# Optimization experiments

Measured on AMD Instinct MI355X. Metric: run time of the kernel, lower is better.

## Reference

```python
import jax, jax.numpy as jnp
import numpy as np

EPS = 1e-5
NEG_SLOPE = 0.1


def _gcn_layer(x, row, col, W, b):
    # GCNConv, improved=True (self-loop weight 2.0), symmetric normalization.
    N = x.shape[0]
    xw = x @ W                                   # [N, H]
    ew = jnp.ones(row.shape[0], dtype=x.dtype)   # edge_weight=None -> ones
    deg = jax.ops.segment_sum(ew, col, num_segments=N) + 2.0  # +2 from improved self loop
    dinv = jax.lax.rsqrt(deg)                    # deg >= 2, always finite
    norm = dinv[row] * dinv[col]                 # [E]
    agg = jax.ops.segment_sum(norm[:, None] * xw[row], col, num_segments=N)
    agg = agg + (2.0 * dinv * dinv)[:, None] * xw  # self-loop contribution
    return agg + b


def _batchnorm(x, w, b):
    # training-mode BN over node dim (biased variance), eps=1e-5
    mu = jnp.mean(x, axis=0)
    var = jnp.mean((x - mu) ** 2, axis=0)
    return (x - mu) * jax.lax.rsqrt(var + EPS) * w + b


def setup_inputs() -> dict:
    key = jax.random.key(0)
    ks = jax.random.split(key, 10)
    N, E, F, H, OUT, G = 100000, 800000, 128, 128, 128, 2048
    x = jax.random.normal(ks[0], (N, F), dtype=jnp.float32)
    edge_index = jax.random.randint(ks[1], (2, E), 0, N, dtype=jnp.int64)
    batch = jnp.sort(jax.random.randint(ks[2], (N,), 0, G, dtype=jnp.int64))
    s1 = 1.0 / np.sqrt(F)
    s2 = 1.0 / np.sqrt(H)
    return {
        "x": x,
        "edge_index": edge_index,
        "batch": batch,
        "W1": jax.random.uniform(ks[3], (F, H), jnp.float32, -s1, s1),
        "b1": jnp.zeros((H,), jnp.float32),
        "bn1_w": jnp.ones((H,), jnp.float32),
        "bn1_b": jnp.zeros((H,), jnp.float32),
        "W2": jax.random.uniform(ks[4], (H, H), jnp.float32, -s2, s2),
        "b2": jnp.zeros((H,), jnp.float32),
        "bn2_w": jnp.ones((H,), jnp.float32),
        "bn2_b": jnp.zeros((H,), jnp.float32),
        "Wf": jax.random.uniform(ks[5], (H, OUT), jnp.float32, -s2, s2),
        "bf": jax.random.uniform(ks[6], (OUT,), jnp.float32, -s2, s2),
        "num_graphs": G,
    }


def reference(x, edge_index, batch, W1, b1, bn1_w, bn1_b, W2, b2, bn2_w, bn2_b, Wf, bf, num_graphs):
    row, col = edge_index[0], edge_index[1]
    h = _gcn_layer(x, row, col, W1, b1)
    h = jax.nn.leaky_relu(_batchnorm(h, bn1_w, bn1_b), NEG_SLOPE)
    # dropout omitted (deterministic reference / eval mode)
    h = _gcn_layer(h, row, col, W2, b2)
    h = jax.nn.leaky_relu(_batchnorm(h, bn2_w, bn2_b), NEG_SLOPE)
    pooled = jax.ops.segment_max(h, batch, num_segments=num_graphs)  # [G, H]
    pooled = jnp.where(jnp.isneginf(pooled), 0.0, pooled)            # empty graphs -> 0
    return pooled @ Wf + bf
```

## Files before the change

### kernel.cpp

```cpp
#include <hip/hip_runtime.h>
#include <hip/hip_bf16.h>

#define EPSV 1e-5f
#define SLOPE 0.1f

typedef __attribute__((ext_vector_type(8))) unsigned short ushort8v;

static __device__ inline unsigned short f2bf(float f) {
    __hip_bfloat16 b = __float2bfloat16(f);
    return *reinterpret_cast<unsigned short*>(&b);
}
static __device__ inline float bf2f(unsigned short u) {
    return __uint_as_float(((unsigned)u) << 16);
}

__global__ __launch_bounds__(256) void k_count(const int* __restrict__ col,
                                               unsigned* __restrict__ cnt, int E) {
    int e = blockIdx.x * 256 + threadIdx.x;
    if (e < E) atomicAdd(&cnt[col[e]], 1u);
}

__global__ __launch_bounds__(256) void k_dinv(const unsigned* __restrict__ cnt,
                                              float* __restrict__ dinv, int N) {
    int n = blockIdx.x * 256 + threadIdx.x;
    if (n < N) dinv[n] = rsqrtf((float)cnt[n] + 2.0f);
}

__global__ __launch_bounds__(256) void k_chunk_sum(const unsigned* __restrict__ cnt, int N,
                                                   unsigned* __restrict__ bsum) {
    __shared__ unsigned ls[256];
    int base = blockIdx.x * 1024;
    unsigned s = 0;
    for (int i = threadIdx.x; i < 1024; i += 256) {
        int idx = base + i;
        if (idx < N) s += cnt[idx];
    }
    ls[threadIdx.x] = s;
    __syncthreads();
    for (int st = 128; st > 0; st >>= 1) {
        if (threadIdx.x < st) ls[threadIdx.x] += ls[threadIdx.x + st];
        __syncthreads();
    }
    if (threadIdx.x == 0) bsum[blockIdx.x] = ls[0];
}

__global__ void k_scan_bsum(unsigned* __restrict__ bsum, int nb) {
    if (threadIdx.x == 0 && blockIdx.x == 0) {
        unsigned acc = 0;
        for (int i = 0; i < nb; i++) { unsigned v = bsum[i]; bsum[i] = acc; acc += v; }
    }
}

__global__ __launch_bounds__(256) void k_scan_chunks(const unsigned* __restrict__ cnt, int N,
                                                     const unsigned* __restrict__ bsum,
                                                     int* __restrict__ off, int E) {
    __shared__ unsigned ls[256];
    int base = blockIdx.x * 1024;
    unsigned v[4];
    unsigned s = 0;
#pragma unroll
    for (int j = 0; j < 4; j++) {
        int idx = base + threadIdx.x * 4 + j;
        v[j] = (idx < N) ? cnt[idx] : 0u;
        s += v[j];
    }
    ls[threadIdx.x] = s;
    __syncthreads();
    if (threadIdx.x == 0) {
        unsigned acc = bsum[blockIdx.x];
        for (int i = 0; i < 256; i++) { unsigned t = ls[i]; ls[i] = acc; acc += t; }
    }
    __syncthreads();
    unsigned acc = ls[threadIdx.x];
#pragma unroll
    for (int j = 0; j < 4; j++) {
        int idx = base + threadIdx.x * 4 + j;
        if (idx < N) off[idx] = (int)acc;
        acc += v[j];
    }
    if (base + threadIdx.x * 4 <= N - 1 && N - 1 < base + threadIdx.x * 4 + 4) off[N] = E;
}

__global__ __launch_bounds__(256) void k_place(const int* __restrict__ row,
                                               const int* __restrict__ col,
                                               const float* __restrict__ dinv,
                                               int* __restrict__ cursor,
                                               int2* __restrict__ spack, int E) {
    int e = blockIdx.x * 256 + threadIdx.x;
    if (e >= E) return;
    int r = row[e], c = col[e];
    int pos = atomicAdd(&cursor[c], 1);
    spack[pos] = make_int2(r, __float_as_int(dinv[r] * dinv[c]));
}

template <int MODE>
__global__ __launch_bounds__(256) void k_gemm_t(const float* __restrict__ X,
                                                const float* __restrict__ W,
                                                const float* __restrict__ sums, float invN,
                                                const float* __restrict__ bnw,
                                                const float* __restrict__ bnb,
                                                const float* __restrict__ bias,
                                                void* __restrict__ Yv, int N) {
    __shared__ float xs[64][132];
    __shared__ float sc[128], sb[128];
    const int tid = threadIdx.x;
    if (MODE == 1) {
        if (tid < 128) {
            float mu = sums[tid] * invN;
            float var = sums[128 + tid] * invN - mu * mu;
            float s = rsqrtf(var + EPSV) * bnw[tid];
            sc[tid] = s;
            sb[tid] = bnb[tid] - mu * s;
        }
        __syncthreads();
    }
    const int base = blockIdx.x * 64;
    for (int i = tid; i < 2048; i += 256) {
        int r = i >> 5, c4 = i & 31;
        int row = base + r; if (row >= N) row = N - 1;
        float4 v = ((const float4*)(X + (size_t)row * 128))[c4];
        if (MODE == 1) {
            int f = c4 * 4;
            v.x = fmaf(v.x, sc[f + 0], sb[f + 0]); v.x = v.x > 0.f ? v.x : SLOPE * v.x;
            v.y = fmaf(v.y, sc[f + 1], sb[f + 1]); v.y = v.y > 0.f ? v.y : SLOPE * v.y;
            v.z = fmaf(v.z, sc[f + 2], sb[f + 2]); v.z = v.z > 0.f ? v.z : SLOPE * v.z;
            v.w = fmaf(v.w, sc[f + 3], sb[f + 3]); v.w = v.w > 0.f ? v.w : SLOPE * v.w;
        }
        *(float4*)(&xs[r][c4 * 4]) = v;
    }
    __syncthreads();
    const int c0 = (tid & 31) * 4;
    const int rg = tid >> 5;
    float acc[8][4];
#pragma unroll
    for (int i = 0; i < 8; i++) { acc[i][0] = acc[i][1] = acc[i][2] = acc[i][3] = 0.f; }
    for (int k = 0; k < 128; k += 4) {
        float4 w0 = *(const float4*)(W + (size_t)(k + 0) * 128 + c0);
        float4 w1 = *(const float4*)(W + (size_t)(k + 1) * 128 + c0);
        float4 w2 = *(const float4*)(W + (size_t)(k + 2) * 128 + c0);
        float4 w3 = *(const float4*)(W + (size_t)(k + 3) * 128 + c0);
#pragma unroll
        for (int i = 0; i < 8; i++) {
            float4 a = *(const float4*)(&xs[rg + 8 * i][k]);
            acc[i][0] = fmaf(a.x, w0.x, fmaf(a.y, w1.x, fmaf(a.z, w2.x, fmaf(a.w, w3.x, acc[i][0]))));
            acc[i][1] = fmaf(a.x, w0.y, fmaf(a.y, w1.y, fmaf(a.z, w2.y, fmaf(a.w, w3.y, acc[i][1]))));
            acc[i][2] = fmaf(a.x, w0.z, fmaf(a.y, w1.z, fmaf(a.z, w2.z, fmaf(a.w, w3.z, acc[i][2]))));
            acc[i][3] = fmaf(a.x, w0.w, fmaf(a.y, w1.w, fmaf(a.z, w2.w, fmaf(a.w, w3.w, acc[i][3]))));
        }
    }
#pragma unroll
    for (int i = 0; i < 8; i++) {
        int row = base + rg + 8 * i;
        if (row < N) {
            if (MODE == 2) {
                float4 o = make_float4(acc[i][0] + bias[c0], acc[i][1] + bias[c0 + 1],
                                       acc[i][2] + bias[c0 + 2], acc[i][3] + bias[c0 + 3]);
                ((float4*)((float*)Yv + (size_t)row * 128))[tid & 31] = o;
            } else {
                ushort4 o;
                o.x = f2bf(acc[i][0]); o.y = f2bf(acc[i][1]);
                o.z = f2bf(acc[i][2]); o.w = f2bf(acc[i][3]);
                ((ushort4*)((unsigned short*)Yv + (size_t)row * 128))[tid & 31] = o;
            }
        }
    }
}

__global__ __launch_bounds__(256) void k_agg2(const unsigned short* __restrict__ xwh,
                                              const int* __restrict__ off,
                                              const int2* __restrict__ spack,
                                              const float* __restrict__ dinv,
                                              const float* __restrict__ bias,
                                              float* __restrict__ h,
                                              float* __restrict__ sums, int N) {
    __shared__ float ls1[128], ls2[128];
    const int tid = threadIdx.x;
    if (tid < 128) { ls1[tid] = 0.f; ls2[tid] = 0.f; }
    __syncthreads();

    const int lane = tid & 63;
    const int q = lane & 15;
    const int g = lane >> 4;
    const int wave = blockIdx.x * 4 + (tid >> 6);
    const int nW = gridDim.x * 4;

    float st1[8] = {0, 0, 0, 0, 0, 0, 0, 0};
    float st2[8] = {0, 0, 0, 0, 0, 0, 0, 0};
    float bj[8];
#pragma unroll
    for (int j = 0; j < 8; j++) bj[j] = bias[q * 8 + j];

    for (int n = wave; n < N; n += nW) {
        int s = off[n], e = off[n + 1];
        float a[8] = {0, 0, 0, 0, 0, 0, 0, 0};
        int i = s + g;
        if (i < e) {
            int2 p = spack[i];
            while (true) {
                int inext = i + 4;
                bool more = inext < e;
                int2 pn = make_int2(0, 0);
                if (more) pn = spack[inext];
                float nm = __int_as_float(p.y);
                ushort8v v = *(const ushort8v*)(xwh + (size_t)p.x * 128 + q * 8);
#pragma unroll
                for (int j = 0; j < 8; j++) a[j] = fmaf(nm, bf2f(v[j]), a[j]);
                if (!more) break;
                p = pn; i = inext;
            }
        }
#pragma unroll
        for (int j = 0; j < 8; j++) {
            a[j] += __shfl_xor(a[j], 16);
            a[j] += __shfl_xor(a[j], 32);
        }
        if (lane < 16) {
            float dc = dinv[n];
            float sl = 2.f * dc * dc;
            ushort8v xv = *(const ushort8v*)(xwh + (size_t)n * 128 + q * 8);
            float o[8];
#pragma unroll
            for (int j = 0; j < 8; j++) {
                o[j] = a[j] + sl * bf2f(xv[j]) + bj[j];
                st1[j] += o[j];
                st2[j] += o[j] * o[j];
            }
            float4* hp = (float4*)(h + (size_t)n * 128 + q * 8);
            hp[0] = make_float4(o[0], o[1], o[2], o[3]);
            hp[1] = make_float4(o[4], o[5], o[6], o[7]);
        }
    }
    if (lane < 16) {
#pragma unroll
        for (int j = 0; j < 8; j++) {
            atomicAdd(&ls1[q * 8 + j], st1[j]);
            atomicAdd(&ls2[q * 8 + j], st2[j]);
        }
    }
    __syncthreads();
    if (tid < 128) {
        atomicAdd(&sums[tid], ls1[tid]);
        atomicAdd(&sums[128 + tid], ls2[tid]);
    }
}

__global__ __launch_bounds__(256) void k_pool_init(unsigned* __restrict__ p, int total) {
    int i = blockIdx.x * 256 + threadIdx.x;
    if (i < total) p[i] = 0x007FFFFFu;
}

__device__ inline unsigned enc_f(float x) {
    unsigned u = __float_as_uint(x);
    return (u & 0x80000000u) ? ~u : (u | 0x80000000u);
}

__global__ __launch_bounds__(256) void k_pool2(const float* __restrict__ h,
                                               const int* __restrict__ batch,
                                               const float* __restrict__ sums, float invN,
                                               const float* __restrict__ bnw,
                                               const float* __restrict__ bnb,
                                               unsigned* __restrict__ pooled, int N) {
    const int f = threadIdx.x & 127;
    const int half = threadIdx.x >> 7;
    float mu = sums[f] * invN;
    float var = sums[128 + f] * invN - mu * mu;
    float scale = rsqrtf(var + EPSV) * bnw[f];
    float bias = bnb[f] - mu * scale;
    const int base = blockIdx.x * 128;
    const int end = min(base + 128, N);
    float m = -__builtin_inff();
    int g = -1;
    for (int n = base + half; n < end; n += 2) {
        int bg = batch[n];
        if (bg != g) {
            if (g >= 0) atomicMax(&pooled[(size_t)g * 128 + f], enc_f(m));
            g = bg;
            m = -__builtin_inff();
        }
        float v = fmaf(h[(size_t)n * 128 + f], scale, bias);
        v = v > 0.f ? v : SLOPE * v;
        m = fmaxf(m, v);
    }
    if (g >= 0) atomicMax(&pooled[(size_t)g * 128 + f], enc_f(m));
}

__global__ __launch_bounds__(256) void k_decode(unsigned* __restrict__ p, int total) {
    int i = blockIdx.x * 256 + threadIdx.x;
    if (i >= total) return;
    unsigned u = p[i];
    float v;
    if (u == 0x007FFFFFu) v = 0.f;
    else if (u & 0x80000000u) v = __uint_as_float(u & 0x7FFFFFFFu);
    else v = __uint_as_float(~u);
    p[i] = __float_as_uint(v);
}

extern "C" void kernel_launch(void* const* d_in, const int* in_sizes, int n_in,
                              void* d_out, int out_size, void* d_ws, size_t ws_size,
                              hipStream_t stream) {
    const float* x     = (const float*)d_in[0];
    const int*   ei    = (const int*)d_in[1];
    const int*   batch = (const int*)d_in[2];
    const float* W1    = (const float*)d_in[3];
    const float* b1    = (const float*)d_in[4];
    const float* bn1w  = (const float*)d_in[5];
    const float* bn1b  = (const float*)d_in[6];
    const float* W2    = (const float*)d_in[7];
    const float* b2    = (const float*)d_in[8];
    const float* bn2w  = (const float*)d_in[9];
    const float* bn2b  = (const float*)d_in[10];
    const float* Wf    = (const float*)d_in[11];
    const float* bf    = (const float*)d_in[12];

    const int N = in_sizes[0] / 128;
    const int E = in_sizes[1] / 2;
    const int G = out_size / 128;
    const int* rowp = ei;
    const int* colp = ei + E;
    float* out = (float*)d_out;
    const float invN = 1.0f / N;

    char* w = (char*)d_ws;
    unsigned short* bufAh = (unsigned short*)w; w += (size_t)N * 128 * 2;
    float*    bufB   = (float*)w;    w += (size_t)N * 128 * 4;
    float*    dinv   = (float*)w;    w += (size_t)N * 4;
    unsigned* cnt    = (unsigned*)w; w += (size_t)N * 4;
    int*      off    = (int*)w;      w += (size_t)(N + 1) * 4;
    unsigned* bsum   = (unsigned*)w; w += 1024 * 4;
    int2*     spack  = (int2*)w;     w += (size_t)E * 8;
    float*    sums   = (float*)w;    w += 512 * 4;
    unsigned* pooled = (unsigned*)w; w += (size_t)G * 128 * 4;

    float* sums1 = sums;
    float* sums2 = sums + 256;
    const int nb = (N + 1023) / 1024;

    hipMemsetAsync(cnt, 0, (size_t)N * 4, stream);
    hipMemsetAsync(sums, 0, 512 * 4, stream);
    k_count<<<(E + 255) / 256, 256, 0, stream>>>(colp, cnt, E);
    k_dinv<<<(N + 255) / 256, 256, 0, stream>>>(cnt, dinv, N);
    k_chunk_sum<<<nb, 256, 0, stream>>>(cnt, N, bsum);
    k_scan_bsum<<<1, 64, 0, stream>>>(bsum, nb);
    k_scan_chunks<<<nb, 256, 0, stream>>>(cnt, N, bsum, off, E);
    hipMemcpyAsync(cnt, off, (size_t)N * 4, hipMemcpyDeviceToDevice, stream);
    k_place<<<(E + 255) / 256, 256, 0, stream>>>(rowp, colp, dinv, (int*)cnt, spack, E);

    k_gemm_t<0><<<(N + 63) / 64, 256, 0, stream>>>(x, W1, nullptr, 0.f, nullptr, nullptr,
                                                   nullptr, bufAh, N);
    k_agg2<<<2048, 256, 0, stream>>>(bufAh, off, spack, dinv, b1, bufB, sums1, N);

    k_gemm_t<1><<<(N + 63) / 64, 256, 0, stream>>>(bufB, W2, sums1, invN, bn1w, bn1b,
                                                   nullptr, bufAh, N);
    k_agg2<<<2048, 256, 0, stream>>>(bufAh, off, spack, dinv, b2, bufB, sums2, N);

    k_pool_init<<<(G * 128 + 255) / 256, 256, 0, stream>>>(pooled, G * 128);
    k_pool2<<<(N + 127) / 128, 256, 0, stream>>>(bufB, batch, sums2, invN, bn2w, bn2b,
                                                 pooled, N);
    k_decode<<<(G * 128 + 255) / 256, 256, 0, stream>>>(pooled, G * 128);

    k_gemm_t<2><<<(G + 63) / 64, 256, 0, stream>>>((const float*)pooled, Wf, nullptr, 0.f,
                                                   nullptr, nullptr, bf, out, G);
}
```

Baseline: 507.3 us.

## Aggregate edges per node-block with shared-memory atomics instead of wave-per-node

Replaces the wave-per-node gather aggregation with a block-per-64-nodes scheme. Each block streams its whole contiguous CSR edge range in 16-edge groups and accumulates into a 64x128 LDS tile using workgroup-scope float atomics. A second pass in the same block adds the self-loop and bias, writes h and reduces BN statistics. This balances work across edges regardless of per-node degree and removes the per-node shuffle reduction. In exchange it doubles the packed edge record to 16 bytes to carry the destination node, adds LDS atomic contention, and uses 32KB of shared memory per block, which limits occupancy.

```diff
diff --git a/kernel.cpp b/kernel.cpp
--- a/kernel.cpp
+++ b/kernel.cpp
@@ -3,6 +3,7 @@
 
 #define EPSV 1e-5f
 #define SLOPE 0.1f
+#define NB 64
 
 typedef __attribute__((ext_vector_type(8))) unsigned short ushort8v;
 
@@ -85,12 +86,12 @@
                                                const int* __restrict__ col,
                                                const float* __restrict__ dinv,
                                                int* __restrict__ cursor,
-                                               int2* __restrict__ spack, int E) {
+                                               int4* __restrict__ spack, int E) {
     int e = blockIdx.x * 256 + threadIdx.x;
     if (e >= E) return;
     int r = row[e], c = col[e];
     int pos = atomicAdd(&cursor[c], 1);
-    spack[pos] = make_int2(r, __float_as_int(dinv[r] * dinv[c]));
+    spack[pos] = make_int4(r, __float_as_int(dinv[r] * dinv[c]), c, 0);
 }
 
 template <int MODE>
@@ -166,81 +167,69 @@
     }
 }
 
-__global__ __launch_bounds__(256) void k_agg2(const unsigned short* __restrict__ xwh,
+__global__ __launch_bounds__(256) void k_agg3(const unsigned short* __restrict__ xwh,
                                               const int* __restrict__ off,
-                                              const int2* __restrict__ spack,
+                                              const int4* __restrict__ spack,
                                               const float* __restrict__ dinv,
                                               const float* __restrict__ bias,
                                               float* __restrict__ h,
                                               float* __restrict__ sums, int N) {
-    __shared__ float ls1[128], ls2[128];
+    __shared__ float acc[NB * 128];
+    __shared__ float ls1[256], ls2[256];
     const int tid = threadIdx.x;
-    if (tid < 128) { ls1[tid] = 0.f; ls2[tid] = 0.f; }
-    __syncthreads();
-
-    const int lane = tid & 63;
-    const int q = lane & 15;
-    const int g = lane >> 4;
-    const int wave = blockIdx.x * 4 + (tid >> 6);
-    const int nW = gridDim.x * 4;
-
-    float st1[8] = {0, 0, 0, 0, 0, 0, 0, 0};
-    float st2[8] = {0, 0, 0, 0, 0, 0, 0, 0};
-    float bj[8];
-#pragma unroll
-    for (int j = 0; j < 8; j++) bj[j] = bias[q * 8 + j];
-
-    for (int n = wave; n < N; n += nW) {
-        int s = off[n], e = off[n + 1];
-        float a[8] = {0, 0, 0, 0, 0, 0, 0, 0};
-        int i = s + g;
-        if (i < e) {
-            int2 p = spack[i];
-            while (true) {
-                int inext = i + 4;
-                bool more = inext < e;
-                int2 pn = make_int2(0, 0);
-                if (more) pn = spack[inext];
-                float nm = __int_as_float(p.y);
-                ushort8v v = *(const ushort8v*)(xwh + (size_t)p.x * 128 + q * 8);
-#pragma unroll
-                for (int j = 0; j < 8; j++) a[j] = fmaf(nm, bf2f(v[j]), a[j]);
-                if (!more) break;
-                p = pn; i = inext;
+    const int n0 = blockIdx.x * NB;
+    const int nEnd = min(n0 + NB, N);
+    for (int i = tid; i < NB * 128; i += 256) acc[i] = 0.f;
+    __syncthreads();
+
+    const int eBeg = off[n0], eEnd = off[nEnd];
+    const int q = tid & 15;
+    const int g = tid >> 4;
+
+    int i = eBeg + g;
+    if (i < eEnd) {
+        int4 p = spack[i];
+        ushort8v v = *(const ushort8v*)(xwh + (size_t)p.x * 128 + q * 8);
+        for (i += 16; i < eEnd; i += 16) {
+            int4 pn = spack[i];
+            ushort8v vn = *(const ushort8v*)(xwh + (size_t)pn.x * 128 + q * 8);
+            float nm = __int_as_float(p.y);
+            float* dst = acc + (p.z - n0) * 128 + q * 8;
+#pragma unroll
+            for (int j = 0; j < 8; j++) {
+                int jj = (j + q) & 7;
+                __hip_atomic_fetch_add(dst + jj, nm * bf2f(v[jj]),
+                                       __ATOMIC_RELAXED, __HIP_MEMORY_SCOPE_WORKGROUP);
             }
-        }
+            p = pn; v = vn;
+        }
+        float nm = __int_as_float(p.y);
+        float* dst = acc + (p.z - n0) * 128 + q * 8;
 #pragma unroll
         for (int j = 0; j < 8; j++) {
-            a[j] += __shfl_xor(a[j], 16);
-            a[j] += __shfl_xor(a[j], 32);
-        }
-        if (lane < 16) {
-            float dc = dinv[n];
-            float sl = 2.f * dc * dc;
-            ushort8v xv = *(const ushort8v*)(xwh + (size_t)n * 128 + q * 8);
-            float o[8];
-#pragma unroll
-            for (int j = 0; j < 8; j++) {
-                o[j] = a[j] + sl * bf2f(xv[j]) + bj[j];
-                st1[j] += o[j];
-                st2[j] += o[j] * o[j];
-            }
-            float4* hp = (float4*)(h + (size_t)n * 128 + q * 8);
-            hp[0] = make_float4(o[0], o[1], o[2], o[3]);
-            hp[1] = make_float4(o[4], o[5], o[6], o[7]);
-        }
-    }
-    if (lane < 16) {
-#pragma unroll
-        for (int j = 0; j < 8; j++) {
-            atomicAdd(&ls1[q * 8 + j], st1[j]);
-            atomicAdd(&ls2[q * 8 + j], st2[j]);
-        }
-    }
+            int jj = (j + q) & 7;
+            __hip_atomic_fetch_add(dst + jj, nm * bf2f(v[jj]),
+                                   __ATOMIC_RELAXED, __HIP_MEMORY_SCOPE_WORKGROUP);
+        }
+    }
+    __syncthreads();
+
+    const int f = tid & 127;
+    const float bj = bias[f];
+    float s1 = 0.f, s2 = 0.f;
+    for (int idx = tid; idx < (nEnd - n0) * 128; idx += 256) {
+        int node = n0 + (idx >> 7);
+        float d = dinv[node];
+        float xv = bf2f(xwh[(size_t)node * 128 + f]);
+        float o = acc[idx] + 2.f * d * d * xv + bj;
+        h[(size_t)node * 128 + f] = o;
+        s1 += o; s2 += o * o;
+    }
+    ls1[tid] = s1; ls2[tid] = s2;
     __syncthreads();
     if (tid < 128) {
-        atomicAdd(&sums[tid], ls1[tid]);
-        atomicAdd(&sums[128 + tid], ls2[tid]);
+        atomicAdd(&sums[f], ls1[tid] + ls1[tid + 128]);
+        atomicAdd(&sums[128 + f], ls2[tid] + ls2[tid + 128]);
     }
 }
 
@@ -325,9 +314,9 @@
     float*    bufB   = (float*)w;    w += (size_t)N * 128 * 4;
     float*    dinv   = (float*)w;    w += (size_t)N * 4;
     unsigned* cnt    = (unsigned*)w; w += (size_t)N * 4;
-    int*      off    = (int*)w;      w += (size_t)(N + 1) * 4;
+    int*      off    = (int*)w;      w += (size_t)(N + 4) * 4;
     unsigned* bsum   = (unsigned*)w; w += 1024 * 4;
-    int2*     spack  = (int2*)w;     w += (size_t)E * 8;
+    int4*     spack  = (int4*)w;     w += (size_t)E * 16;
     float*    sums   = (float*)w;    w += 512 * 4;
     unsigned* pooled = (unsigned*)w; w += (size_t)G * 128 * 4;
 
@@ -345,13 +334,15 @@
     hipMemcpyAsync(cnt, off, (size_t)N * 4, hipMemcpyDeviceToDevice, stream);
     k_place<<<(E + 255) / 256, 256, 0, stream>>>(rowp, colp, dinv, (int*)cnt, spack, E);
 
+    const int aggGrid = (N + NB - 1) / NB;
+
     k_gemm_t<0><<<(N + 63) / 64, 256, 0, stream>>>(x, W1, nullptr, 0.f, nullptr, nullptr,
                                                    nullptr, bufAh, N);
-    k_agg2<<<2048, 256, 0, stream>>>(bufAh, off, spack, dinv, b1, bufB, sums1, N);
+    k_agg3<<<aggGrid, 256, 0, stream>>>(bufAh, off, spack, dinv, b1, bufB, sums1, N);
 
     k_gemm_t<1><<<(N + 63) / 64, 256, 0, stream>>>(bufB, W2, sums1, invN, bn1w, bn1b,
                                                    nullptr, bufAh, N);
-    k_agg2<<<2048, 256, 0, stream>>>(bufAh, off, spack, dinv, b2, bufB, sums2, N);
+    k_agg3<<<aggGrid, 256, 0, stream>>>(bufAh, off, spack, dinv, b2, bufB, sums2, N);
 
     k_pool_init<<<(G * 128 + 255) / 256, 256, 0, stream>>>(pooled, G * 128);
     k_pool2<<<(N + 127) / 128, 256, 0, stream>>>(bufB, batch, sums2, invN, bn2w, bn2b,
```

Result: slower. 1.445 ms (+184.9%).

## Assign one 16-lane group per node in aggregation with 8-way unrolled gathers

Applied to the files above, without the earlier changes.

The aggregation kernel now maps each destination node to a 16-thread group instead of a full 64-lane wave. Each group walks all of the node's edges itself, with the loop unrolled by 8 and then 4 so several independent gathers are in flight at once. This removes the cross-lane shuffle reduction and the idle lanes during the epilogue, and puts four nodes in each wave. In exchange it uses more registers, and load balance across lanes within a wave now depends on how degrees vary between neighbouring nodes.

```diff
diff --git a/kernel.cpp b/kernel.cpp
--- a/kernel.cpp
+++ b/kernel.cpp
@@ -166,7 +166,7 @@
     }
 }
 
-__global__ __launch_bounds__(256) void k_agg2(const unsigned short* __restrict__ xwh,
+__global__ __launch_bounds__(256) void k_agg5(const unsigned short* __restrict__ xwh,
                                               const int* __restrict__ off,
                                               const int2* __restrict__ spack,
                                               const float* __restrict__ dinv,
@@ -178,64 +178,83 @@
     if (tid < 128) { ls1[tid] = 0.f; ls2[tid] = 0.f; }
     __syncthreads();
 
-    const int lane = tid & 63;
-    const int q = lane & 15;
-    const int g = lane >> 4;
-    const int wave = blockIdx.x * 4 + (tid >> 6);
-    const int nW = gridDim.x * 4;
-
+    const int q = tid & 15;
+    const int grp = (blockIdx.x * 256 + tid) >> 4;
+    const int nGrp = gridDim.x * 16;
+
+    float bj[8];
+#pragma unroll
+    for (int j = 0; j < 8; j++) bj[j] = bias[q * 8 + j];
     float st1[8] = {0, 0, 0, 0, 0, 0, 0, 0};
     float st2[8] = {0, 0, 0, 0, 0, 0, 0, 0};
-    float bj[8];
-#pragma unroll
-    for (int j = 0; j < 8; j++) bj[j] = bias[q * 8 + j];
-
-    for (int n = wave; n < N; n += nW) {
-        int s = off[n], e = off[n + 1];
+
+    for (int n = grp; n < N; n += nGrp) {
+        const int s = off[n], e = off[n + 1];
         float a[8] = {0, 0, 0, 0, 0, 0, 0, 0};
-        int i = s + g;
-        if (i < e) {
+        int i = s;
+        for (; i + 8 <= e; i += 8) {
+            int2 p0 = spack[i + 0], p1 = spack[i + 1], p2 = spack[i + 2], p3 = spack[i + 3];
+            int2 p4 = spack[i + 4], p5 = spack[i + 5], p6 = spack[i + 6], p7 = spack[i + 7];
+            ushort8v v0 = *(const ushort8v*)(xwh + (size_t)p0.x * 128 + q * 8);
+            ushort8v v1 = *(const ushort8v*)(xwh + (size_t)p1.x * 128 + q * 8);
+            ushort8v v2 = *(const ushort8v*)(xwh + (size_t)p2.x * 128 + q * 8);
+            ushort8v v3 = *(const ushort8v*)(xwh + (size_t)p3.x * 128 + q * 8);
+            ushort8v v4 = *(const ushort8v*)(xwh + (size_t)p4.x * 128 + q * 8);
+            ushort8v v5 = *(const ushort8v*)(xwh + (size_t)p5.x * 128 + q * 8);
+            ushort8v v6 = *(const ushort8v*)(xwh + (size_t)p6.x * 128 + q * 8);
+            ushort8v v7 = *(const ushort8v*)(xwh + (size_t)p7.x * 128 + q * 8);
+            float n0 = __int_as_float(p0.y), n1 = __int_as_float(p1.y);
+            float n2 = __int_as_float(p2.y), n3 = __int_as_float(p3.y);
+            float n4 = __int_as_float(p4.y), n5 = __int_as_float(p5.y);
+            float n6 = __int_as_float(p6.y), n7 = __int_as_float(p7.y);
+#pragma unroll
+            for (int j = 0; j < 8; j++) {
+                float t = fmaf(n0, bf2f(v0[j]), fmaf(n1, bf2f(v1[j]),
+                          fmaf(n2, bf2f(v2[j]), n3 * bf2f(v3[j]))));
+                float u = fmaf(n4, bf2f(v4[j]), fmaf(n5, bf2f(v5[j]),
+                          fmaf(n6, bf2f(v6[j]), n7 * bf2f(v7[j]))));
+                a[j] += t + u;
+            }
+        }
+        for (; i + 4 <= e; i += 4) {
+            int2 p0 = spack[i + 0], p1 = spack[i + 1], p2 = spack[i + 2], p3 = spack[i + 3];
+            ushort8v v0 = *(const ushort8v*)(xwh + (size_t)p0.x * 128 + q * 8);
+            ushort8v v1 = *(const ushort8v*)(xwh + (size_t)p1.x * 128 + q * 8);
+            ushort8v v2 = *(const ushort8v*)(xwh + (size_t)p2.x * 128 + q * 8);
+            ushort8v v3 = *(const ushort8v*)(xwh + (size_t)p3.x * 128 + q * 8);
+            float n0 = __int_as_float(p0.y), n1 = __int_as_float(p1.y);
+            float n2 = __int_as_float(p2.y), n3 = __int_as_float(p3.y);
+#pragma unroll
+            for (int j = 0; j < 8; j++) {
+                a[j] += fmaf(n0, bf2f(v0[j]), fmaf(n1, bf2f(v1[j]),
+                        fmaf(n2, bf2f(v2[j]), n3 * bf2f(v3[j]))));
+            }
+        }
+        for (; i < e; ++i) {
             int2 p = spack[i];
-            while (true) {
-                int inext = i + 4;
-                bool more = inext < e;
-                int2 pn = make_int2(0, 0);
-                if (more) pn = spack[inext];
-                float nm = __int_as_float(p.y);
-                ushort8v v = *(const ushort8v*)(xwh + (size_t)p.x * 128 + q * 8);
-#pragma unroll
-                for (int j = 0; j < 8; j++) a[j] = fmaf(nm, bf2f(v[j]), a[j]);
-                if (!more) break;
-                p = pn; i = inext;
-            }
-        }
+            ushort8v v = *(const ushort8v*)(xwh + (size_t)p.x * 128 + q * 8);
+            float nm = __int_as_float(p.y);
+#pragma unroll
+            for (int j = 0; j < 8; j++) a[j] = fmaf(nm, bf2f(v[j]), a[j]);
+        }
+        float dc = dinv[n];
+        float sl = 2.f * dc * dc;
+        ushort8v xv = *(const ushort8v*)(xwh + (size_t)n * 128 + q * 8);
+        float o[8];
 #pragma unroll
         for (int j = 0; j < 8; j++) {
-            a[j] += __shfl_xor(a[j], 16);
-            a[j] += __shfl_xor(a[j], 32);
-        }
-        if (lane < 16) {
-            float dc = dinv[n];
-            float sl = 2.f * dc * dc;
-            ushort8v xv = *(const ushort8v*)(xwh + (size_t)n * 128 + q * 8);
-            float o[8];
-#pragma unroll
-            for (int j = 0; j < 8; j++) {
-                o[j] = a[j] + sl * bf2f(xv[j]) + bj[j];
-                st1[j] += o[j];
-                st2[j] += o[j] * o[j];
-            }
-            float4* hp = (float4*)(h + (size_t)n * 128 + q * 8);
-            hp[0] = make_float4(o[0], o[1], o[2], o[3]);
-            hp[1] = make_float4(o[4], o[5], o[6], o[7]);
-        }
-    }
-    if (lane < 16) {
-#pragma unroll
-        for (int j = 0; j < 8; j++) {
-            atomicAdd(&ls1[q * 8 + j], st1[j]);
-            atomicAdd(&ls2[q * 8 + j], st2[j]);
-        }
+            o[j] = fmaf(sl, bf2f(xv[j]), a[j]) + bj[j];
+            st1[j] += o[j];
+            st2[j] += o[j] * o[j];
+        }
+        float4* hp = (float4*)(h + (size_t)n * 128 + q * 8);
+        hp[0] = make_float4(o[0], o[1], o[2], o[3]);
+        hp[1] = make_float4(o[4], o[5], o[6], o[7]);
+    }
+#pragma unroll
+    for (int j = 0; j < 8; j++) {
+        atomicAdd(&ls1[q * 8 + j], st1[j]);
+        atomicAdd(&ls2[q * 8 + j], st2[j]);
     }
     __syncthreads();
     if (tid < 128) {
@@ -325,7 +344,7 @@
     float*    bufB   = (float*)w;    w += (size_t)N * 128 * 4;
     float*    dinv   = (float*)w;    w += (size_t)N * 4;
     unsigned* cnt    = (unsigned*)w; w += (size_t)N * 4;
-    int*      off    = (int*)w;      w += (size_t)(N + 1) * 4;
+    int*      off    = (int*)w;      w += (size_t)(N + 4) * 4;
     unsigned* bsum   = (unsigned*)w; w += 1024 * 4;
     int2*     spack  = (int2*)w;     w += (size_t)E * 8;
     float*    sums   = (float*)w;    w += 512 * 4;
@@ -345,13 +364,15 @@
     hipMemcpyAsync(cnt, off, (size_t)N * 4, hipMemcpyDeviceToDevice, stream);
     k_place<<<(E + 255) / 256, 256, 0, stream>>>(rowp, colp, dinv, (int*)cnt, spack, E);
 
+    const int aggBlocks = 2048;
+
     k_gemm_t<0><<<(N + 63) / 64, 256, 0, stream>>>(x, W1, nullptr, 0.f, nullptr, nullptr,
                                                    nullptr, bufAh, N);
-    k_agg2<<<2048, 256, 0, stream>>>(bufAh, off, spack, dinv, b1, bufB, sums1, N);
+    k_agg5<<<aggBlocks, 256, 0, stream>>>(bufAh, off, spack, dinv, b1, bufB, sums1, N);
 
     k_gemm_t<1><<<(N + 63) / 64, 256, 0, stream>>>(bufB, W2, sums1, invN, bn1w, bn1b,
                                                    nullptr, bufAh, N);
-    k_agg2<<<2048, 256, 0, stream>>>(bufAh, off, spack, dinv, b2, bufB, sums2, N);
+    k_agg5<<<aggBlocks, 256, 0, stream>>>(bufAh, off, spack, dinv, b2, bufB, sums2, N);
 
     k_pool_init<<<(G * 128 + 255) / 256, 256, 0, stream>>>(pooled, G * 128);
     k_pool2<<<(N + 127) / 128, 256, 0, stream>>>(bufB, batch, sums2, invN, bn2w, bn2b,
```

After: 497.2 us. 1.02x faster.
